# Kernel tuning notes

Hardware: AMD Instinct MI355X
Metric: run time of the kernel (lower is better)

The kernel has to match this reference:

```python
import jax, jax.numpy as jnp
import numpy as np

BASE = 10000.0

def _rope(x):
    # x: [b, n, h, d]; positions along token axis n, rotate-half convention
    d = x.shape[-1]
    n = x.shape[1]
    inv_freq = 1.0 / (BASE ** (jnp.arange(0, d, 2, dtype=jnp.float32) / d))  # [d/2]
    t = jnp.arange(n, dtype=jnp.float32)
    freqs = jnp.outer(t, inv_freq)                       # [n, d/2]
    emb = jnp.concatenate([freqs, freqs], axis=-1)       # [n, d]
    cos = jnp.cos(emb)[None, :, None, :]
    sin = jnp.sin(emb)[None, :, None, :]
    x1, x2 = jnp.split(x, 2, axis=-1)
    rot = jnp.concatenate([-x2, x1], axis=-1)
    return x * cos + rot * sin


def setup_inputs() -> dict:
    key = jax.random.key(0)
    k1, k2, k3 = jax.random.split(key, 3)
    b, c, hh, ww = 64, 1024, 16, 16
    x = jax.random.normal(k1, (b, c, hh, ww), dtype=jnp.float32)
    w_qkv = jax.random.normal(k2, (3 * c, c), dtype=jnp.float32) * 0.02
    w_lin = jax.random.normal(k3, (c, c, 1, 1), dtype=jnp.float32) * 0.02
    b_lin = jnp.zeros((c,), dtype=jnp.float32)
    return {"x": x, "w_qkv": w_qkv, "w_lin": w_lin, "b_lin": b_lin, "n_heads": 16}


def reference(x, w_qkv, w_lin, b_lin, n_heads):
    b, c, hh, ww = x.shape
    n = hh * ww
    d_head = c // n_heads
    scale = d_head ** -0.5
    # flatten(2).transpose(-2,-1): [b, n, c]
    xt = jnp.transpose(x.reshape(b, c, n), (0, 2, 1))
    # qkv proj, unflatten to [b, n, heads, 3*d_head], chunk along last dim
    qkv = (xt @ w_qkv.T).reshape(b, n, n_heads, 3 * d_head)
    q, k, v = jnp.split(qkv, 3, axis=-1)                  # each [b, n, h, d]
    q = _rope(q)
    k = _rope(k)
    q = jax.nn.softmax(q, axis=-1) * scale                # softmax over d_head
    k = jax.nn.softmax(k, axis=-2)                        # softmax over heads axis (as in torch code)
    # k^T @ v over the heads axis -> per-token [d_head, d_head] context
    context = jnp.einsum('bnhd,bnhe->bnde', k, v)
    o = jnp.einsum('bnhd,bnde->bnhe', q, context)         # [b, n, h, d]
    # transpose(-2,-1).reshape(b, c, h, w)
    o = jnp.transpose(o, (0, 1, 3, 2)).reshape(b, c, hh, ww)
    # 1x1 conv
    return jnp.einsum('bchw,oc->bohw', o, w_lin[:, :, 0, 0]) + b_lin[None, :, None, None]
```

## Files before the change

kernel.cpp:

```cpp
#include <hip/hip_runtime.h>
#include <hip/hip_bf16.h>
#include <math.h>

typedef __hip_bfloat16 hbf16;
typedef __attribute__((ext_vector_type(8))) __bf16    bf16x8;
typedef __attribute__((ext_vector_type(4))) float     f32x4;
typedef __attribute__((ext_vector_type(4))) _Float16  f16x4;
typedef __attribute__((ext_vector_type(8))) unsigned short u16x8;

#define C_    1024
#define NTOK  256
#define NH    16
#define J3    3072

__device__ __forceinline__ unsigned short fbits(float v){
    return __builtin_bit_cast(unsigned short, __float2bfloat16(v));
}
__device__ __forceinline__ __bf16 to_bf(float v){
    return __builtin_bit_cast(__bf16, __float2bfloat16(v));
}

__device__ __forceinline__ void gload_lds16(const __bf16* g, __bf16* l) {
    __builtin_amdgcn_global_load_lds((const __attribute__((address_space(1))) void*)g,
                                     (__attribute__((address_space(3))) void*)l, 16, 0, 0);
}

__global__ __launch_bounds__(256) void cvt_w(const float* __restrict__ wq,
                                             __bf16* __restrict__ wqo,
                                             const float* __restrict__ wl,
                                             __bf16* __restrict__ wlo) {
    const float* in; __bf16* out; int i;
    if (blockIdx.x < 3072) { in = wq; out = wqo; i = blockIdx.x * 256 + threadIdx.x; }
    else                   { in = wl; out = wlo; i = (blockIdx.x - 3072) * 256 + threadIdx.x; }
    float4 v = ((const float4*)in)[i];
    ushort4 u;
    u.x = fbits(v.x); u.y = fbits(v.y); u.z = fbits(v.z); u.w = fbits(v.w);
    ((ushort4*)out)[i] = u;
}

__global__ __launch_bounds__(256) void xpose_x(const float* __restrict__ X,
                                               __bf16* __restrict__ Xt) {
    __shared__ float t[32][36];
    const int b = blockIdx.z, k0 = blockIdx.y * 32, s0 = blockIdx.x * 32;
    const int tid = threadIdx.x;
    {
        int kl = tid >> 3, s4 = (tid & 7) * 4;
        float4 v = *(const float4*)(X + ((size_t)b << 18) + (size_t)(k0 + kl) * 256 + s0 + s4);
        t[kl][s4] = v.x; t[kl][s4 + 1] = v.y; t[kl][s4 + 2] = v.z; t[kl][s4 + 3] = v.w;
    }
    __syncthreads();
    {
        int sl = tid >> 3, k4 = (tid & 7) * 4;
        ushort4 u;
        u.x = fbits(t[k4][sl]); u.y = fbits(t[k4 + 1][sl]);
        u.z = fbits(t[k4 + 2][sl]); u.w = fbits(t[k4 + 3][sl]);
        *(ushort4*)(Xt + (size_t)(b * 256 + s0 + sl) * 1024 + k0 + k4) = u;
    }
}

#define WAITVM(N) asm volatile("s_waitcnt vmcnt(" #N ")" ::: "memory")

__device__ __forceinline__ void stage_tile(const __bf16* __restrict__ Ag,
                                           const __bf16* __restrict__ Bg,
                                           __bf16* sa, __bf16* sb,
                                           int kk, int wave, int lane) {
    const int rl = lane >> 2;
    const int cg = (lane & 3) ^ ((lane >> 3) & 3);
    const int coff = kk + cg * 8;
    #pragma unroll
    for (int i = 0; i < 2; ++i) {
        const int seg = wave * 2 + i;
        const int row = seg * 16 + rl;
        gload_lds16(Ag + ((size_t)row << 10) + coff, sa + seg * 512);
        gload_lds16(Bg + ((size_t)row << 10) + coff, sb + seg * 512);
    }
}

#define GBODY(BT, NBUF, T, DOSTG, DOPF, CA, CB, NA, NB)                        \
  {                                                                            \
    asm volatile("s_waitcnt vmcnt(0)" ::: "memory");                           \
    __builtin_amdgcn_s_barrier();                                              \
    __builtin_amdgcn_sched_barrier(0);                                         \
    if (DOSTG) stage_tile(Ab, Bb, sm.kl.A + (((BT) + 2) % 3) * 8192,           \
                          sm.kl.B + (((BT) + 2) % 3) * 8192, ((T) + 2) << 5,   \
                          wave, lane);                                         \
    bf16x8 h1[4];                                                              \
    {                                                                          \
      const __bf16* sa_ = sm.kl.A + (BT) * 8192 + aoff;                        \
      _Pragma("unroll") for (int mi = 0; mi < 4; ++mi)                         \
          h1[mi] = *(const bf16x8*)(sa_ + (mi + 4) * 512);                     \
    }                                                                          \
    if (DOPF) {                                                                \
      const __bf16* na_ = sm.kl.A + (NBUF) * 8192 + aoff;                      \
      const __bf16* nb_ = sm.kl.B + (NBUF) * 8192 + boff;                      \
      _Pragma("unroll") for (int i = 0; i < 4; ++i) {                          \
        NA[i] = *(const bf16x8*)(na_ + i * 512);                               \
        NB[i] = *(const bf16x8*)(nb_ + i * 512);                               \
      }                                                                        \
    }                                                                          \
    __builtin_amdgcn_s_setprio(1);                                             \
    _Pragma("unroll") for (int mi = 0; mi < 4; ++mi)                           \
      _Pragma("unroll") for (int ni = 0; ni < 4; ++ni)                         \
        acc[mi][ni] = __builtin_amdgcn_mfma_f32_16x16x32_bf16(                 \
            CA[mi], CB[ni], acc[mi][ni], 0, 0, 0);                             \
    _Pragma("unroll") for (int mi = 0; mi < 4; ++mi)                           \
      _Pragma("unroll") for (int ni = 0; ni < 4; ++ni)                         \
        acc[mi + 4][ni] = __builtin_amdgcn_mfma_f32_16x16x32_bf16(             \
            h1[mi], CB[ni], acc[mi + 4][ni], 0, 0, 0);                         \
    __builtin_amdgcn_s_setprio(0);                                             \
  }

template <int EPI>
__global__ __launch_bounds__(512, 2) void gemm256(const __bf16* __restrict__ A,
                                                  const __bf16* __restrict__ B,
                                                  void* __restrict__ Cout,
                                                  const float* __restrict__ bias) {
    __shared__ union __align__(16) {
        struct { __bf16 A[3 * 8192]; __bf16 B[3 * 8192]; } kl;
        __bf16 st[128][264];
    } sm;

    const int tid  = threadIdx.x;
    const int wave = tid >> 6, lane = tid & 63;
    const int wm = wave >> 2, wn = wave & 3;
    const int quad = lane >> 4, m = lane & 15;

    const int wg = blockIdx.x;
    int mb, nb;
    if (EPI == 0) {
        const int local = wg >> 3;
        mb = (wg & 7) * 8 + (local & 7);
        nb = local >> 3;
    } else {
        const int local = wg >> 3;
        mb = local & 3;
        nb = (wg & 7) * 8 + (local >> 2);
    }
    const int m0 = mb << 8, n0 = nb << 8;

    const __bf16* Ab = A + ((size_t)m0 << 10);
    const __bf16* Bb = B + ((size_t)n0 << 10);

    const int pcs  = quad ^ ((lane >> 1) & 3);
    const int aoff = (wm * 128 + m) * 32 + pcs * 8;
    const int boff = (wn * 64  + m) * 32 + pcs * 8;

    f32x4 acc[8][4] = {};
    bf16x8 p0a[4], p0b[4], p1a[4], p1b[4];

    stage_tile(Ab, Bb, sm.kl.A,        sm.kl.B,        0,  wave, lane);
    stage_tile(Ab, Bb, sm.kl.A + 8192, sm.kl.B + 8192, 32, wave, lane);
    WAITVM(4);
    __builtin_amdgcn_s_barrier();
    __builtin_amdgcn_sched_barrier(0);
    #pragma unroll
    for (int i = 0; i < 4; ++i) {
        p0a[i] = *(const bf16x8*)(sm.kl.A + aoff + i * 512);
        p0b[i] = *(const bf16x8*)(sm.kl.B + boff + i * 512);
    }

    for (int tt = 0; tt < 30; tt += 6) {
        GBODY(0, 1, tt + 0, 1, 1, p0a, p0b, p1a, p1b);
        GBODY(1, 2, tt + 1, 1, 1, p1a, p1b, p0a, p0b);
        GBODY(2, 0, tt + 2, 1, 1, p0a, p0b, p1a, p1b);
        GBODY(0, 1, tt + 3, 1, 1, p1a, p1b, p0a, p0b);
        GBODY(1, 2, tt + 4, 1, 1, p0a, p0b, p1a, p1b);
        GBODY(2, 0, tt + 5, 1, 1, p1a, p1b, p0a, p0b);
    }
    GBODY(0, 1, 30, 0, 1, p0a, p0b, p1a, p1b);
    GBODY(1, 0, 31, 0, 0, p1a, p1b, p0a, p0b);

    if (EPI == 0) {
        __syncthreads();
        __bf16* Y = (__bf16*)Cout;
        #pragma unroll
        for (int h = 0; h < 2; ++h) {
            if (wm == h) {
                #pragma unroll
                for (int mi = 0; mi < 8; ++mi)
                    #pragma unroll
                    for (int ni = 0; ni < 4; ++ni) {
                        const int r = mi * 16 + quad * 4;
                        const int c = wn * 64 + ni * 16 + m;
                        #pragma unroll
                        for (int j = 0; j < 4; ++j)
                            sm.st[r + j][c] = to_bf(acc[mi][ni][j]);
                    }
            }
            __syncthreads();
            #pragma unroll
            for (int i = 0; i < 8; ++i) {
                const int cid = i * 512 + tid;
                const int r = cid >> 5, ch = (cid & 31) * 8;
                *(bf16x8*)(Y + (size_t)(m0 + h * 128 + r) * 3072 + n0 + ch) =
                    *(const bf16x8*)&sm.st[r][ch];
            }
            __syncthreads();
        }
    } else {
        float* outp = (float*)Cout;
        const int cl = lane & 15, rq = lane >> 4;
        const int rbase = m0 + wm * 128 + rq * 4;
        const int nbase = n0 + wn * 64 + cl;
        #pragma unroll
        for (int mi = 0; mi < 8; ++mi) {
            float bia[4];
            #pragma unroll
            for (int j = 0; j < 4; ++j) bia[j] = bias[rbase + mi * 16 + j];
            #pragma unroll
            for (int ni = 0; ni < 4; ++ni) {
                const int nn = nbase + ni * 16;
                const size_t base = ((size_t)(nn >> 8) << 18) + (nn & 255);
                #pragma unroll
                for (int j = 0; j < 4; ++j) {
                    const int oc = rbase + mi * 16 + j;
                    outp[base + ((size_t)oc << 8)] = acc[mi][ni][j] + bia[j];
                }
            }
        }
    }
}

__global__ __launch_bounds__(1024) void attn_mfma(const __bf16* __restrict__ Y,
                                                  __bf16* __restrict__ Ot) {
    __shared__ union __align__(16) {
        __bf16  v[16][1024];
        ushort4 ost[256][16];
    } sm;

    const int tid  = threadIdx.x;
    const int wave = tid >> 6, lane = tid & 63;
    const int bb = blockIdx.x >> 4;
    const int n0 = (blockIdx.x & 15) * 16;
    const int n  = n0 + wave;
    const int quad = lane >> 4, m = lane & 15;
    const __bf16* Yt = Y + (size_t)(bb * 256 + n) * J3;

    #pragma unroll
    for (int p = 0; p < 2; ++p) {
        const int h = p * 8 + (lane >> 3), part = lane & 7;
        gload_lds16(Yt + h * 192 + 128 + part * 8, &sm.v[wave][p * 512]);
    }

    bf16x8 qb[2], kb[2];
    #pragma unroll
    for (int st = 0; st < 2; ++st) {
        qb[st] = *(const bf16x8*)(Yt + m * 192 +      st * 32 + quad * 8);
        kb[st] = *(const bf16x8*)(Yt + m * 192 + 64 + st * 32 + quad * 8);
    }
    float qf[16], kf[16];
    #pragma unroll
    for (int st = 0; st < 2; ++st)
        #pragma unroll
        for (int j = 0; j < 8; ++j) {
            qf[st * 8 + j] = (float)qb[st][j];
            kf[st * 8 + j] = (float)kb[st][j];
        }

    const float fn = (float)n;
    #pragma unroll
    for (int j = 0; j < 8; ++j) {
        const float d  = (float)(quad * 8 + j);
        const float th = fn * __expf(-0.28782313662425572f * d);
        const float sn = __sinf(th), cn = __cosf(th);
        float a0 = qf[j], a1 = qf[8 + j];
        qf[j]     = a0 * cn - a1 * sn;
        qf[8 + j] = a1 * cn + a0 * sn;
        float b0 = kf[j], b1 = kf[8 + j];
        kf[j]     = b0 * cn - b1 * sn;
        kf[8 + j] = b1 * cn + b0 * sn;
    }

    float qe[16], ls = 0.f;
    #pragma unroll
    for (int i = 0; i < 16; ++i) { qe[i] = __expf(qf[i]); ls += qe[i]; }
    ls += __shfl_xor(ls, 16);
    ls += __shfl_xor(ls, 32);
    const float qinv = 0.125f * __builtin_amdgcn_rcpf(ls);
    bf16x8 qbh[2];
    #pragma unroll
    for (int st = 0; st < 2; ++st)
        #pragma unroll
        for (int j = 0; j < 8; ++j) qbh[st][j] = to_bf(qe[st * 8 + j] * qinv);

    float ke[16], kc[16];
    #pragma unroll
    for (int i = 0; i < 16; ++i) { ke[i] = __expf(kf[i]); kc[i] = ke[i]; }
    #pragma unroll
    for (int msk = 1; msk <= 8; msk <<= 1)
        #pragma unroll
        for (int i = 0; i < 16; ++i) kc[i] += __shfl_xor(kc[i], msk);
    bf16x8 kbh[2];
    #pragma unroll
    for (int st = 0; st < 2; ++st)
        #pragma unroll
        for (int j = 0; j < 8; ++j)
            kbh[st][j] = to_bf(ke[st * 8 + j] * __builtin_amdgcn_rcpf(kc[st * 8 + j]));

    f32x4 Sp = {0.f, 0.f, 0.f, 0.f};
    Sp = __builtin_amdgcn_mfma_f32_16x16x32_bf16(kbh[0], qbh[0], Sp, 0, 0, 0);
    Sp = __builtin_amdgcn_mfma_f32_16x16x32_bf16(kbh[1], qbh[1], Sp, 0, 0, 0);

    __syncthreads();

    f32x4 o4[4];
#if __has_builtin(__builtin_amdgcn_mfma_f32_16x16x16f16)
    f16x4 af;
    #pragma unroll
    for (int r = 0; r < 4; ++r) af[r] = (_Float16)Sp[r];
    #pragma unroll
    for (int tile = 0; tile < 4; ++tile) {
        f16x4 bv;
        #pragma unroll
        for (int j = 0; j < 4; ++j)
            bv[j] = (_Float16)(float)sm.v[wave][(quad * 4 + j) * 64 + tile * 16 + m];
        f32x4 z = {0.f, 0.f, 0.f, 0.f};
        o4[tile] = __builtin_amdgcn_mfma_f32_16x16x16f16(af, bv, z, 0, 0, 0);
    }
#else
    bf16x8 a2;
    #pragma unroll
    for (int j = 0; j < 8; ++j) {
        int k = quad * 8 + j;
        int src = ((k & 15) >> 2) * 16 + m;
        float v = __shfl(Sp[k & 3], src, 64);
        a2[j] = (quad < 2) ? to_bf(v) : to_bf(0.f);
    }
    #pragma unroll
    for (int tile = 0; tile < 4; ++tile) {
        bf16x8 bv;
        #pragma unroll
        for (int j = 0; j < 8; ++j) {
            int k = quad * 8 + j;
            int kk = (k < 16) ? k : 0;
            bv[j] = sm.v[wave][kk * 64 + tile * 16 + m];
        }
        f32x4 z = {0.f, 0.f, 0.f, 0.f};
        o4[tile] = __builtin_amdgcn_mfma_f32_16x16x32_bf16(a2, bv, z, 0, 0, 0);
    }
#endif

    __syncthreads();

    #pragma unroll
    for (int r = 0; r < 4; ++r) {
        const int s = m * 16 + quad * 4 + r;
        const int phys = wave ^ (quad * 4 + r) ^ m;
        ushort4 u;
        u.x = fbits(o4[0][r]); u.y = fbits(o4[1][r]);
        u.z = fbits(o4[2][r]); u.w = fbits(o4[3][r]);
        sm.ost[s][phys] = u;
    }
    __syncthreads();

    {
        const int row = tid >> 2;
        const int w0  = (tid & 3) * 4;
        ushort4 u4[4];
        #pragma unroll
        for (int j = 0; j < 4; ++j) {
            const int phys = (w0 + j) ^ (row & 15) ^ (row >> 4);
            u4[j] = sm.ost[row][phys];
        }
        __bf16* dst = Ot + (((size_t)(bb * 256 + row)) << 10) + n0 * 4 + w0 * 4;
        u16x8 a = {u4[0].x, u4[0].y, u4[0].z, u4[0].w, u4[1].x, u4[1].y, u4[1].z, u4[1].w};
        u16x8 b = {u4[2].x, u4[2].y, u4[2].z, u4[2].w, u4[3].x, u4[3].y, u4[3].z, u4[3].w};
        *(u16x8*)dst = a;
        *(u16x8*)(dst + 8) = b;
    }
}

extern "C" void kernel_launch(void* const* d_in, const int* in_sizes, int n_in,
                              void* d_out, int out_size, void* d_ws, size_t ws_size,
                              hipStream_t stream) {
    const float* x     = (const float*)d_in[0];
    const float* w_qkv = (const float*)d_in[1];
    const float* w_lin = (const float*)d_in[2];
    const float* b_lin = (const float*)d_in[3];
    float* out = (float*)d_out;

    char* ws = (char*)d_ws;
    __bf16* Y    = (__bf16*)ws;
    __bf16* XtOt = (__bf16*)(ws + (size_t)100663296);
    __bf16* Wqb  = (__bf16*)(ws + (size_t)134217728);
    __bf16* Wlb  = (__bf16*)(ws + (size_t)140509184);

    cvt_w<<<4096, 256, 0, stream>>>(w_qkv, Wqb, w_lin, Wlb);
    xpose_x<<<dim3(8, 32, 64), 256, 0, stream>>>(x, XtOt);

    gemm256<0><<<768, 512, 0, stream>>>(XtOt, Wqb, (void*)Y, nullptr);
    attn_mfma<<<1024, 1024, 0, stream>>>(Y, XtOt);
    gemm256<1><<<256, 512, 0, stream>>>(Wlb, XtOt, (void*)out, b_lin);
}
```

Measured before the change: 311.6 us.

## Restructure GEMM main loop into 4-stage LDS pipeline with split A/B staging

Replaces the 3-buffer GEMM K-loop, which used register double-buffered fragments and a full vmcnt(0) wait every tile, with a 4-buffer LDS ring that keeps two tiles of global loads in flight. Each step is split into two half-MFMA phases with barriers, and the A and B staging for the tile three ahead is interleaved between them. Fragments are loaded from LDS just before use rather than prefetched into registers a tile early. The aim is deeper latency hiding of global-to-LDS loads and lower register pressure. The cost is more barriers per tile and more LDS, which at the existing two-blocks-per-CU launch bound may limit occupancy.

Measured after the change: 313.1 us. About the same (+0.5%).

```diff
diff --git a/kernel.cpp b/kernel.cpp
--- a/kernel.cpp
+++ b/kernel.cpp
@@ -58,12 +58,11 @@
     }
 }
 
-#define WAITVM(N) asm volatile("s_waitcnt vmcnt(" #N ")" ::: "memory")
-
-__device__ __forceinline__ void stage_tile(const __bf16* __restrict__ Ag,
-                                           const __bf16* __restrict__ Bg,
-                                           __bf16* sa, __bf16* sb,
-                                           int kk, int wave, int lane) {
+#define WAITVM_I(N) asm volatile("s_waitcnt vmcnt(" #N ")" ::: "memory")
+#define WAITVM(N) WAITVM_I(N)
+
+__device__ __forceinline__ void stage_unit(const __bf16* __restrict__ G,
+                                           __bf16* l, int kk, int wave, int lane) {
     const int rl = lane >> 2;
     const int cg = (lane & 3) ^ ((lane >> 3) & 3);
     const int coff = kk + cg * 8;
@@ -71,43 +70,49 @@
     for (int i = 0; i < 2; ++i) {
         const int seg = wave * 2 + i;
         const int row = seg * 16 + rl;
-        gload_lds16(Ag + ((size_t)row << 10) + coff, sa + seg * 512);
-        gload_lds16(Bg + ((size_t)row << 10) + coff, sb + seg * 512);
-    }
-}
-
-#define GBODY(BT, NBUF, T, DOSTG, DOPF, CA, CB, NA, NB)                        \
+        gload_lds16(G + ((size_t)row << 10) + coff, l + seg * 512);
+    }
+}
+
+#define BARRIER()                                                              \
+    __builtin_amdgcn_sched_barrier(0);                                         \
+    __builtin_amdgcn_s_barrier();                                              \
+    __builtin_amdgcn_sched_barrier(0)
+
+#define STEP(BUF, S, DOSTG, VM)                                                \
   {                                                                            \
-    asm volatile("s_waitcnt vmcnt(0)" ::: "memory");                           \
-    __builtin_amdgcn_s_barrier();                                              \
-    __builtin_amdgcn_sched_barrier(0);                                         \
-    if (DOSTG) stage_tile(Ab, Bb, sm.kl.A + (((BT) + 2) % 3) * 8192,           \
-                          sm.kl.B + (((BT) + 2) % 3) * 8192, ((T) + 2) << 5,   \
-                          wave, lane);                                         \
-    bf16x8 h1[4];                                                              \
-    {                                                                          \
-      const __bf16* sa_ = sm.kl.A + (BT) * 8192 + aoff;                        \
-      _Pragma("unroll") for (int mi = 0; mi < 4; ++mi)                         \
-          h1[mi] = *(const bf16x8*)(sa_ + (mi + 4) * 512);                     \
-    }                                                                          \
-    if (DOPF) {                                                                \
-      const __bf16* na_ = sm.kl.A + (NBUF) * 8192 + aoff;                      \
-      const __bf16* nb_ = sm.kl.B + (NBUF) * 8192 + boff;                      \
-      _Pragma("unroll") for (int i = 0; i < 4; ++i) {                          \
-        NA[i] = *(const bf16x8*)(na_ + i * 512);                               \
-        NB[i] = *(const bf16x8*)(nb_ + i * 512);                               \
-      }                                                                        \
-    }                                                                          \
+    const __bf16* sa_ = sm.kl + (BUF) * 16384 + aoff;                          \
+    const __bf16* sb_ = sm.kl + (BUF) * 16384 + 8192 + boff;                   \
+    bf16x8 bfr[4], afr[4];                                                     \
+                               \
+    _Pragma("unroll") for (int ni = 0; ni < 4; ++ni)                           \
+        bfr[ni] = *(const bf16x8*)(sb_ + ni * 512);                            \
+    _Pragma("unroll") for (int mi = 0; mi < 4; ++mi)                           \
+        afr[mi] = *(const bf16x8*)(sa_ + mi * 512);                            \
+    if (DOSTG) stage_unit(Ab, sm.kl + (((S) + 3) & 3) * 16384,                 \
+                          ((S) + 3) << 5, wave, lane);                         \
+    BARRIER();                                                                 \
     __builtin_amdgcn_s_setprio(1);                                             \
     _Pragma("unroll") for (int mi = 0; mi < 4; ++mi)                           \
       _Pragma("unroll") for (int ni = 0; ni < 4; ++ni)                         \
         acc[mi][ni] = __builtin_amdgcn_mfma_f32_16x16x32_bf16(                 \
-            CA[mi], CB[ni], acc[mi][ni], 0, 0, 0);                             \
+            afr[mi], bfr[ni], acc[mi][ni], 0, 0, 0);                           \
+    __builtin_amdgcn_s_setprio(0);                                             \
+    BARRIER();                                                                 \
+                                      \
+    _Pragma("unroll") for (int mi = 0; mi < 4; ++mi)                           \
+        afr[mi] = *(const bf16x8*)(sa_ + (mi + 4) * 512);                      \
+    if (DOSTG) stage_unit(Bb, sm.kl + (((S) + 3) & 3) * 16384 + 8192,          \
+                          ((S) + 3) << 5, wave, lane);                         \
+    BARRIER();                                                                 \
+    __builtin_amdgcn_s_setprio(1);                                             \
     _Pragma("unroll") for (int mi = 0; mi < 4; ++mi)                           \
       _Pragma("unroll") for (int ni = 0; ni < 4; ++ni)                         \
         acc[mi + 4][ni] = __builtin_amdgcn_mfma_f32_16x16x32_bf16(             \
-            h1[mi], CB[ni], acc[mi + 4][ni], 0, 0, 0);                         \
+            afr[mi], bfr[ni], acc[mi + 4][ni], 0, 0, 0);                       \
     __builtin_amdgcn_s_setprio(0);                                             \
+    WAITVM(VM);                                                                \
+    BARRIER();                                                                 \
   }
 
 template <int EPI>
@@ -116,7 +121,7 @@
                                                   void* __restrict__ Cout,
                                                   const float* __restrict__ bias) {
     __shared__ union __align__(16) {
-        struct { __bf16 A[3 * 8192]; __bf16 B[3 * 8192]; } kl;
+        __bf16 kl[4 * 16384];
         __bf16 st[128][264];
     } sm;
 
@@ -146,29 +151,26 @@
     const int boff = (wn * 64  + m) * 32 + pcs * 8;
 
     f32x4 acc[8][4] = {};
-    bf16x8 p0a[4], p0b[4], p1a[4], p1b[4];
-
-    stage_tile(Ab, Bb, sm.kl.A,        sm.kl.B,        0,  wave, lane);
-    stage_tile(Ab, Bb, sm.kl.A + 8192, sm.kl.B + 8192, 32, wave, lane);
-    WAITVM(4);
-    __builtin_amdgcn_s_barrier();
-    __builtin_amdgcn_sched_barrier(0);
-    #pragma unroll
-    for (int i = 0; i < 4; ++i) {
-        p0a[i] = *(const bf16x8*)(sm.kl.A + aoff + i * 512);
-        p0b[i] = *(const bf16x8*)(sm.kl.B + boff + i * 512);
-    }
-
-    for (int tt = 0; tt < 30; tt += 6) {
-        GBODY(0, 1, tt + 0, 1, 1, p0a, p0b, p1a, p1b);
-        GBODY(1, 2, tt + 1, 1, 1, p1a, p1b, p0a, p0b);
-        GBODY(2, 0, tt + 2, 1, 1, p0a, p0b, p1a, p1b);
-        GBODY(0, 1, tt + 3, 1, 1, p1a, p1b, p0a, p0b);
-        GBODY(1, 2, tt + 4, 1, 1, p0a, p0b, p1a, p1b);
-        GBODY(2, 0, tt + 5, 1, 1, p1a, p1b, p0a, p0b);
-    }
-    GBODY(0, 1, 30, 0, 1, p0a, p0b, p1a, p1b);
-    GBODY(1, 0, 31, 0, 0, p1a, p1b, p0a, p0b);
+
+    stage_unit(Ab, sm.kl,                 0,  wave, lane);
+    stage_unit(Bb, sm.kl + 8192,          0,  wave, lane);
+    stage_unit(Ab, sm.kl + 16384,         32, wave, lane);
+    stage_unit(Bb, sm.kl + 16384 + 8192,  32, wave, lane);
+    stage_unit(Ab, sm.kl + 32768,         64, wave, lane);
+    stage_unit(Bb, sm.kl + 32768 + 8192,  64, wave, lane);
+    WAITVM(8);
+    BARRIER();
+
+    for (int tt = 0; tt < 28; tt += 4) {
+        STEP(0, tt + 0, 1, 8)
+        STEP(1, tt + 1, 1, 8)
+        STEP(2, tt + 2, 1, 8)
+        STEP(3, tt + 3, 1, 8)
+    }
+    STEP(0, 28, 1, 8)
+    STEP(1, 29, 0, 4)
+    STEP(2, 30, 0, 0)
+    STEP(3, 31, 0, 0)
 
     if (EPI == 0) {
         __syncthreads();
```
